# Optimization experiments

Hardware: AMD Instinct MI355X
Metric: run time of the kernel (lower is better)

The kernel has to match this reference:

```python
import jax, jax.numpy as jnp
import numpy as np

B, L, D = 4, 2048, 256
EXPAND, D_STATE, D_CONV = 2, 16, 4
D_INNER = EXPAND * D
DT_RANK = (D + 15) // 16  # ceil(d_model/16) = 16
N_HEADS = 4
H_MLP = int(D * 4.0)
EPS = 1e-5


def _ln(x, w, b):
    mu = x.mean(-1, keepdims=True)
    var = ((x - mu) ** 2).mean(-1, keepdims=True)
    return (x - mu) / jnp.sqrt(var + EPS) * w + b


def _silu(x):
    return x * jax.nn.sigmoid(x)


def _mamba(x, Win, convw, convb, Wx, Wdt, bdt, Alog, Dp, Wout):
    # x: (B, L, D) -> (B, L, D). Standard Mamba mixer (selective scan).
    b, l, d = x.shape
    xz = x @ Win.T                      # (b, l, 2*d_inner)
    xi, z = jnp.split(xz, 2, axis=-1)
    # depthwise causal conv1d, kernel D_CONV
    xc = jnp.swapaxes(xi, 1, 2)         # (b, d_inner, l)
    xc = jax.lax.conv_general_dilated(
        xc, convw, (1,), [(D_CONV - 1, 0)],
        feature_group_count=D_INNER, dimension_numbers=('NCW', 'OIW', 'NCW'))
    xi = _silu(jnp.swapaxes(xc + convb[None, :, None], 1, 2))  # (b, l, d_inner)
    dbl = xi @ Wx.T                     # (b, l, dt_rank + 2*d_state)
    dt = jax.nn.softplus(dbl[..., :DT_RANK] @ Wdt.T + bdt)     # (b, l, d_inner)
    Bm = dbl[..., DT_RANK:DT_RANK + D_STATE]                    # (b, l, n)
    Cm = dbl[..., DT_RANK + D_STATE:]                            # (b, l, n)
    A = -jnp.exp(Alog)                  # (d_inner, n)

    def step(h, ins):
        dt_t, B_t, C_t, u_t = ins       # (b,d_inner),(b,n),(b,n),(b,d_inner)
        h = h * jnp.exp(dt_t[..., None] * A) + dt_t[..., None] * B_t[:, None, :] * u_t[..., None]
        return h, jnp.einsum('bdn,bn->bd', h, C_t)

    xs = tuple(jnp.swapaxes(t, 0, 1) for t in (dt, Bm, Cm, xi))  # time-major
    h0 = jnp.zeros((b, D_INNER, D_STATE), x.dtype)
    _, ys = jax.lax.scan(step, h0, xs)  # ys: (l, b, d_inner)
    y = jnp.swapaxes(ys, 0, 1) + xi * Dp
    return (y * _silu(z)) @ Wout.T


def _attn(x, Wqkv, bqkv, Wo, bo):
    b, l, d = x.shape
    hd = d // N_HEADS
    qkv = x @ Wqkv.T + bqkv
    q, k, v = jnp.split(qkv, 3, axis=-1)
    sh = lambda t: t.reshape(b, l, N_HEADS, hd).transpose(0, 2, 1, 3)
    q, k, v = sh(q), sh(k), sh(v)
    a = jax.nn.softmax(jnp.einsum('bhqd,bhkd->bhqk', q, k) / np.float32(np.sqrt(hd)), axis=-1)
    o = jnp.einsum('bhqk,bhkd->bhqd', a, v).transpose(0, 2, 1, 3).reshape(b, l, d)
    return o @ Wo.T + bo


def setup_inputs() -> dict:
    key = jax.random.key(0)
    ks = iter(jax.random.split(key, 40))
    rn = lambda shape, s=0.02: jax.random.normal(next(ks), shape, jnp.float32) * s
    inp = {'x': jax.random.normal(next(ks), (B, L, D), jnp.float32)}
    for p in ('mf', 'mb'):
        inp[p + '_Win'] = rn((2 * D_INNER, D))
        inp[p + '_convw'] = rn((D_INNER, 1, D_CONV), 0.1)
        inp[p + '_convb'] = jnp.zeros((D_INNER,), jnp.float32)
        inp[p + '_Wx'] = rn((DT_RANK + 2 * D_STATE, D_INNER))
        inp[p + '_Wdt'] = rn((D_INNER, DT_RANK), 0.1)
        inp[p + '_bdt'] = rn((D_INNER,), 0.5)
        inp[p + '_Alog'] = jnp.log(jnp.broadcast_to(jnp.arange(1, D_STATE + 1, dtype=jnp.float32), (D_INNER, D_STATE)))
        inp[p + '_D'] = jnp.ones((D_INNER,), jnp.float32)
        inp[p + '_Wout'] = rn((D, D_INNER))
    for n in ('n1', 'n2', 'n3'):
        inp[n + 'w'] = jnp.ones((D,), jnp.float32)
        inp[n + 'b'] = jnp.zeros((D,), jnp.float32)
    inp['Wqkv'] = rn((3 * D, D))
    inp['bqkv'] = jnp.zeros((3 * D,), jnp.float32)
    inp['Wo'] = rn((D, D))
    inp['bo'] = jnp.zeros((D,), jnp.float32)
    inp['fc1w'] = rn((H_MLP, D))
    inp['fc1b'] = jnp.zeros((H_MLP,), jnp.float32)
    inp['fc2w'] = rn((D, H_MLP))
    inp['fc2b'] = jnp.zeros((D,), jnp.float32)
    return inp


def reference(x, n1w, n1b, n2w, n2b, n3w, n3b,
              mf_Win, mf_convw, mf_convb, mf_Wx, mf_Wdt, mf_bdt, mf_Alog, mf_D, mf_Wout,
              mb_Win, mb_convw, mb_convb, mb_Wx, mb_Wdt, mb_bdt, mb_Alog, mb_D, mb_Wout,
              Wqkv, bqkv, Wo, bo, fc1w, fc1b, fc2w, fc2b):
    # Mamba branch (bidirectional): DropPath is identity at eval
    h = _ln(x, n1w, n1b)
    fwd = _mamba(h, mf_Win, mf_convw, mf_convb, mf_Wx, mf_Wdt, mf_bdt, mf_Alog, mf_D, mf_Wout)
    bwd = jnp.flip(_mamba(jnp.flip(h, 1), mb_Win, mb_convw, mb_convb, mb_Wx, mb_Wdt, mb_bdt, mb_Alog, mb_D, mb_Wout), 1)
    x = x + fwd + bwd
    # Attention branch (full attention since window=None)
    x = x + _attn(_ln(x, n2w, n2b), Wqkv, bqkv, Wo, bo)
    # MLP branch (exact GELU like torch default)
    h = _ln(x, n3w, n3b)
    x = x + (jax.nn.gelu(h @ fc1w.T + fc1b, approximate=False) @ fc2w.T + fc2b)
    return x
```

## Files before the change

### kernel.cpp

```cpp
#include <hip/hip_runtime.h>
#include <hip/hip_bf16.h>
#include <math.h>

#define LL 2048
#define DD 256
#define MTOT 8192
#define DINNER 512
#define CT 32
#define NC 64

typedef __attribute__((ext_vector_type(8))) short short8;
typedef __attribute__((ext_vector_type(4))) float f32x4;

__device__ __forceinline__ float us2f(unsigned short u){
  return __uint_as_float(((unsigned)u) << 16);
}
__device__ __forceinline__ unsigned short f2us(float f){
  __hip_bfloat16 h = __float2bfloat16(f);
  return *(unsigned short*)&h;
}

__global__ void probe_kernel(const unsigned* __restrict__ alog, int* __restrict__ flag){
  if (threadIdx.x == 0 && blockIdx.x == 0) *flag = (alog[0] != 0u) ? 1 : 0;
}

struct Srcs { const void* p[32]; unsigned off[33]; unsigned foff[32]; };

__global__ __launch_bounds__(256) void cvt_all_kernel(Srcs s, float* __restrict__ dst,
                                                      unsigned short* __restrict__ db,
                                                      const int* __restrict__ flag,
                                                      unsigned total){
  unsigned i = blockIdx.x * 256u + threadIdx.x;
  if (i >= total) return;
  int k = 31;
  while (s.off[k] > i) --k;
  unsigned j = i - s.off[k];
  float v;
  if (*flag) v = us2f(((const unsigned short*)s.p[k])[j]);
  else       v = ((const float*)s.p[k])[j];
  if ((k == 24 && j < 65536u) || (k == 25 && j < 256u)) v *= 0.125f;
  db[i] = f2us(v);
  if (s.foff[k] != 0xFFFFFFFFu) dst[s.foff[k] + j] = v;
}

__global__ __launch_bounds__(256) void cvt_x_kernel(const void* __restrict__ src,
                                                    float* __restrict__ dst,
                                                    const int* __restrict__ flag, unsigned n){
  unsigned i = blockIdx.x * 256u + threadIdx.x;
  if (i >= n) return;
  if (*flag) dst[i] = us2f(((const unsigned short*)src)[i]);
  else       dst[i] = ((const float*)src)[i];
}

__global__ __launch_bounds__(256) void wc_prep_kernel(
    const float* __restrict__ Wdt, int dsWdt,
    const float* __restrict__ Wx, int dsWx,
    unsigned short* __restrict__ Wc)
{
  const unsigned g = blockIdx.x * 256u + threadIdx.x;
  const int dir = g >> 18;
  const unsigned idx = g & 262143u;
  const int n = idx >> 9, k = idx & 511;
  const float* wd = Wdt + (size_t)dir * dsWdt + n * 16;
  const float* wx = Wx + (size_t)dir * dsWx + k;
  float s = 0.f;
  #pragma unroll
  for (int j = 0; j < 16; ++j) s = fmaf(wd[j], wx[(size_t)j * 512], s);
  Wc[g] = f2us(s);
}

__global__ __launch_bounds__(256) void final_out_kernel(
    const float* __restrict__ xf, void* __restrict__ out,
    const int* __restrict__ flag, unsigned n)
{
  unsigned i = blockIdx.x * 256u + threadIdx.x;
  if (i >= n) return;
  float v = xf[i];
  if (*flag) ((unsigned short*)out)[i] = f2us(v);
  else       ((float*)out)[i] = v;
}

enum { G_BF16=0, G_GELU=1, G_RESID=2 };
__global__ __launch_bounds__(256) void gemm_mfma_kernel(
    const unsigned short* __restrict__ A, int lda, int agap,
    const unsigned short* __restrict__ W, const unsigned short* __restrict__ W2,
    int Kw, int nsplit, int ksplit,
    const float* __restrict__ bias,
    unsigned short* __restrict__ Cb, float* __restrict__ resid,
    int N, int K, int kslices, int mode)
{
  __shared__ unsigned short sA[64][40];
  __shared__ unsigned short sW[64][40];
  const int tid = threadIdx.x;
  const int w = tid >> 6, lane = tid & 63, quad = lane >> 4, l16 = lane & 15;
  const int m0 = blockIdx.y << 6, n0 = blockIdx.x << 6;
  const int ks = blockIdx.z;
  const int kper = K / kslices;
  const int srow = tid >> 2, skc = (tid & 3) << 3;
  int wr = n0 + srow;
  const unsigned short* Wbase = W;
  if (nsplit && wr >= nsplit){ Wbase = W2; wr -= nsplit; }
  f32x4 acc[4] = {};
  for (int k0 = ks * kper; k0 < ks * kper + kper; k0 += 32){
    int ac = k0 + skc;
    if (agap && ac >= 512) ac += 512;
    short8 av = *(const short8*)(A + (size_t)(m0 + srow) * lda + ac);
    int kk = k0 + skc;
    const unsigned short* Wp = Wbase;
    if (ksplit && kk >= ksplit){ Wp = W2; kk -= ksplit; }
    short8 wv = *(const short8*)(Wp + (size_t)wr * Kw + kk);
    __syncthreads();
    *(short8*)&sA[srow][skc] = av;
    *(short8*)&sW[srow][skc] = wv;
    __syncthreads();
    short8 af = *(const short8*)&sA[w * 16 + l16][quad << 3];
    #pragma unroll
    for (int ns = 0; ns < 4; ++ns){
      short8 wf = *(const short8*)&sW[ns * 16 + l16][quad << 3];
      acc[ns] = __builtin_amdgcn_mfma_f32_16x16x32_bf16(af, wf, acc[ns], 0, 0, 0);
    }
  }
  #pragma unroll
  for (int ns = 0; ns < 4; ++ns){
    const int n = n0 + ns * 16 + l16;
    const float bv = (bias && (mode != G_RESID || ks == 0)) ? bias[n] : 0.f;
    #pragma unroll
    for (int r = 0; r < 4; ++r){
      const int m = m0 + w * 16 + quad * 4 + r;
      const size_t off = (size_t)m * N + n;
      float v = acc[ns][r] + bv;
      if (mode == G_BF16) Cb[off] = f2us(v);
      else if (mode == G_GELU) Cb[off] = f2us(0.5f * v * (1.f + erff(v * 0.70710678118f)));
      else atomicAdd(resid + off, v);
    }
  }
}

__global__ __launch_bounds__(256) void dtbc_mfma_kernel(
    const unsigned short* __restrict__ xi,
    const unsigned short* __restrict__ Wc,
    const unsigned short* __restrict__ WxBCf,
    const unsigned short* __restrict__ WxBCb,
    const float* __restrict__ bdt0, int dsBdt,
    unsigned short* __restrict__ dt16,
    float* __restrict__ dblBC)
{
  __shared__ unsigned short sA[64][40];
  __shared__ unsigned short sW[64][40];
  const int tid = threadIdx.x;
  const int w = tid >> 6, lane = tid & 63, quad = lane >> 4, l16 = lane & 15;
  const int bx = blockIdx.x, m0 = blockIdx.y << 6, dir = blockIdx.z;
  const bool isBC = (bx == 8);
  const unsigned short* A = xi + (size_t)dir * 4194304;
  const unsigned short* W;
  if (isBC) W = dir ? WxBCb : WxBCf;
  else      W = Wc + (size_t)dir * 262144 + ((size_t)bx << 6) * 512;
  const int srow = tid >> 2, skc = (tid & 3) << 3;
  const int wrow = isBC ? (srow & 31) : srow;
  f32x4 acc[4] = {};
  for (int k0 = 0; k0 < 512; k0 += 32){
    short8 av = *(const short8*)(A + (size_t)(m0 + srow) * 512 + k0 + skc);
    short8 wv = *(const short8*)(W + (size_t)wrow * 512 + k0 + skc);
    __syncthreads();
    *(short8*)&sA[srow][skc] = av;
    *(short8*)&sW[srow][skc] = wv;
    __syncthreads();
    short8 af = *(const short8*)&sA[w * 16 + l16][quad << 3];
    #pragma unroll
    for (int ns = 0; ns < 4; ++ns){
      short8 wf = *(const short8*)&sW[ns * 16 + l16][quad << 3];
      acc[ns] = __builtin_amdgcn_mfma_f32_16x16x32_bf16(af, wf, acc[ns], 0, 0, 0);
    }
  }
  #pragma unroll
  for (int ns = 0; ns < 4; ++ns){
    const int nl = ns * 16 + l16;
    #pragma unroll
    for (int r = 0; r < 4; ++r){
      const int m = m0 + w * 16 + quad * 4 + r;
      float v = acc[ns][r];
      if (!isBC){
        const int n = (bx << 6) + nl;
        v += (bdt0 + (size_t)dir * dsBdt)[n];
        float sp = (v > 20.f) ? v : log1pf(__expf(v));
        dt16[(size_t)dir * 4194304 + (size_t)m * 512 + n] = f2us(sp);
      } else if (nl < 32){
        dblBC[(size_t)dir * 262144 + (size_t)m * 32 + nl] = v;
      }
    }
  }
}

__global__ __launch_bounds__(256) void ln_kernel(
    const float* __restrict__ xin,
    const float* __restrict__ w, const float* __restrict__ b,
    unsigned short* __restrict__ hout)
{
  const int row = blockIdx.x, tid = threadIdx.x;
  const size_t off = (size_t)row * DD + tid;
  float v = xin[off];
  float s = v, s2 = v * v;
  #pragma unroll
  for (int o = 32; o; o >>= 1){ s += __shfl_xor(s, o); s2 += __shfl_xor(s2, o); }
  __shared__ float ls[4], ls2[4];
  if ((tid & 63) == 0){ ls[tid >> 6] = s; ls2[tid >> 6] = s2; }
  __syncthreads();
  s  = ls[0] + ls[1] + ls[2] + ls[3];
  s2 = ls2[0] + ls2[1] + ls2[2] + ls2[3];
  const float mu  = s * (1.f / DD);
  const float var = s2 * (1.f / DD) - mu * mu;
  const float inv = rsqrtf(var + 1e-5f);
  hout[off] = f2us((v - mu) * inv * w[tid] + b[tid]);
}

__global__ __launch_bounds__(256) void conv_silu_kernel(
    const unsigned short* __restrict__ xzc, const float* __restrict__ convw0, int dsCw,
    const float* __restrict__ convb0, int dsCb, unsigned short* __restrict__ xi)
{
  const unsigned idx = blockIdx.x * 256u + threadIdx.x;
  const int c = idx & 511;
  const int t = (idx >> 9) & 2047;
  const int b = (idx >> 20) & 3;
  const int dir = idx >> 22;
  const float* cw = convw0 + (size_t)dir * dsCw;
  float acc = (convb0 + (size_t)dir * dsCb)[c];
  if (!dir){
    #pragma unroll
    for (int k = 0; k < 4; ++k){
      int tt = t - 3 + k;
      if (tt >= 0) acc += cw[c*4 + k] * us2f(xzc[((size_t)(b*2048 + tt))*2048 + c]);
    }
  } else {
    #pragma unroll
    for (int j = 0; j < 4; ++j){
      int tt = t + j;
      if (tt < 2048) acc += cw[c*4 + 3 - j] * us2f(xzc[((size_t)(b*2048 + tt))*2048 + 1024 + c]);
    }
  }
  xi[(size_t)dir * 4194304 + ((size_t)(b*2048 + t))*512 + c] = f2us(acc / (1.f + __expf(-acc)));
}

__global__ __launch_bounds__(256) void scan_part1_kernel(
    const unsigned short* __restrict__ dtb, int dsDt,
    const unsigned short* __restrict__ xib, int dsXi,
    const float* __restrict__ dblb, int dsDbl,
    const float* __restrict__ Alog, int dsAl,
    float* __restrict__ dtsum, int dsDts,
    float* __restrict__ hend, int dsHend)
{
  const int bx = blockIdx.x;
  const int dg = bx & 1, c = (bx >> 1) & (NC - 1), b = (bx >> 7) & 3, dir = bx >> 9;
  const int tid = threadIdx.x;
  const int d = dg * 256 + tid;
  const unsigned short* dt_ = dtb + (size_t)dir * dsDt;
  const unsigned short* xi_ = xib + (size_t)dir * dsXi;
  const float* db_ = dblb + (size_t)dir * dsDbl;
  const float* Al_ = Alog + (size_t)dir * dsAl;
  __shared__ float sB[CT][16];
  for (int i = tid; i < CT * 16; i += 256){
    const int s = i >> 4, nn = i & 15;
    const int t = dir ? (LL - 1 - (c * CT + s)) : (c * CT + s);
    sB[s][nn] = db_[(size_t)(b * LL + t) * 32 + nn];
  }
  float A[16];
  #pragma unroll
  for (int n = 0; n < 16; ++n) A[n] = -__expf(Al_[d * 16 + n]);
  __syncthreads();
  float h[16];
  #pragma unroll
  for (int n = 0; n < 16; ++n) h[n] = 0.f;
  float dts = 0.f;
  for (int s = 0; s < CT; ++s){
    const int t = dir ? (LL - 1 - (c * CT + s)) : (c * CT + s);
    const size_t row = (size_t)(b * LL + t);
    const float dtv = us2f(dt_[row * 512 + d]);
    const float uv  = us2f(xi_[row * 512 + d]);
    const float dtu = dtv * uv;
    dts += dtv;
    float bl[16];
    #pragma unroll
    for (int q = 0; q < 4; ++q) *(float4*)&bl[q * 4] = *(const float4*)&sB[s][q * 4];
    #pragma unroll
    for (int n = 0; n < 16; ++n){
      const float e = __expf(dtv * A[n]);
      h[n] = h[n] * e + dtu * bl[n];
    }
  }
  const size_t base = (size_t)dir * dsHend + ((size_t)((b * NC + c) * 512 + d)) * 16;
  #pragma unroll
  for (int q = 0; q < 4; ++q) *(float4*)&hend[base + q * 4] = *(const float4*)&h[q * 4];
  dtsum[(size_t)dir * dsDts + (size_t)(b * NC + c) * 512 + d] = dts;
}

__global__ __launch_bounds__(256) void scan_combine_kernel(
    const float* __restrict__ dtsum, int dsDts,
    float* __restrict__ hend, int dsHend,
    const float* __restrict__ Alog, int dsAl)
{
  const unsigned g = blockIdx.x * 256u + threadIdx.x;
  const int dir = g >> 15;
  const unsigned gg = g & 32767u;
  const int b = gg >> 13, d = (gg >> 4) & 511, n = gg & 15;
  const float A = -__expf((Alog + (size_t)dir * dsAl)[d * 16 + n]);
  const float* dts_ = dtsum + (size_t)dir * dsDts;
  float* he_ = hend + (size_t)dir * dsHend;
  float h = 0.f;
  for (int c = 0; c < NC; ++c){
    const size_t sb = ((size_t)((b * NC + c) * 512 + d)) * 16 + n;
    const float e = __expf(dts_[(size_t)(b * NC + c) * 512 + d] * A);
    const float he = he_[sb];
    he_[sb] = h;
    h = h * e + he;
  }
}

__global__ __launch_bounds__(256) void scan_part2_kernel(
    const unsigned short* __restrict__ dtb, int dsDt,
    const unsigned short* __restrict__ xib, int dsXi,
    const float* __restrict__ dblb, int dsDbl,
    unsigned short* __restrict__ xzc,
    const float* __restrict__ Alog, int dsAl,
    const float* __restrict__ Dp, int dsD,
    const float* __restrict__ hin, int dsHend)
{
  const int bx = blockIdx.x;
  const int dg = bx & 1, c = (bx >> 1) & (NC - 1), b = (bx >> 7) & 3, dir = bx >> 9;
  const int tid = threadIdx.x;
  const int d = dg * 256 + tid;
  const unsigned short* dt_ = dtb + (size_t)dir * dsDt;
  const unsigned short* xi_ = xib + (size_t)dir * dsXi;
  const float* db_ = dblb + (size_t)dir * dsDbl;
  const float* Al_ = Alog + (size_t)dir * dsAl;
  __shared__ float sB[CT][16];
  __shared__ float sC[CT][16];
  for (int i = tid; i < CT * 16; i += 256){
    const int s = i >> 4, nn = i & 15;
    const int t = dir ? (LL - 1 - (c * CT + s)) : (c * CT + s);
    sB[s][nn] = db_[(size_t)(b * LL + t) * 32 + nn];
    sC[s][nn] = db_[(size_t)(b * LL + t) * 32 + 16 + nn];
  }
  float A[16];
  #pragma unroll
  for (int n = 0; n < 16; ++n) A[n] = -__expf(Al_[d * 16 + n]);
  const float Dv = (Dp + (size_t)dir * dsD)[d];
  __syncthreads();
  float h[16];
  const size_t base = (size_t)dir * dsHend + ((size_t)((b * NC + c) * 512 + d)) * 16;
  #pragma unroll
  for (int q = 0; q < 4; ++q) *(float4*)&h[q * 4] = *(const float4*)&hin[base + q * 4];
  for (int s = 0; s < CT; ++s){
    const int t = dir ? (LL - 1 - (c * CT + s)) : (c * CT + s);
    const size_t row = (size_t)(b * LL + t);
    const float dtv = us2f(dt_[row * 512 + d]);
    const float uv  = us2f(xi_[row * 512 + d]);
    const float dtu = dtv * uv;
    float bl[16], cl[16];
    #pragma unroll
    for (int q = 0; q < 4; ++q){
      *(float4*)&bl[q * 4] = *(const float4*)&sB[s][q * 4];
      *(float4*)&cl[q * 4] = *(const float4*)&sC[s][q * 4];
    }
    float p = uv * Dv;
    #pragma unroll
    for (int n = 0; n < 16; ++n){
      const float e = __expf(dtv * A[n]);
      h[n] = h[n] * e + dtu * bl[n];
      p = fmaf(h[n], cl[n], p);
    }
    const float z = us2f(xzc[row * 2048 + dir * 1024 + 512 + d]);
    xzc[row * 2048 + dir * 1024 + d] = f2us(p * (z / (1.f + __expf(-z))));
  }
}

__global__ __launch_bounds__(256) void v_prep_kernel(
    const unsigned short* __restrict__ qkvb, unsigned short* __restrict__ Vt)
{
  const int kt = blockIdx.x;
  const int bh = blockIdx.y;
  const int b = bh >> 2, h = bh & 3;
  __shared__ unsigned short tile[64][72];
  #pragma unroll
  for (int rr = 0; rr < 4; ++rr){
    const int idx = (rr * 256 + threadIdx.x) * 4;
    const int key = idx >> 6, d = idx & 63;
    ushort4 v = *(const ushort4*)(qkvb + ((size_t)(b * 2048 + kt * 64 + key)) * 768 + 512 + h * 64 + d);
    *(ushort4*)&tile[key][d] = v;
  }
  __syncthreads();
  #pragma unroll
  for (int rr = 0; rr < 8; ++rr){
    const int o2 = rr * 256 + threadIdx.x;
    const int d = o2 >> 5, k2 = (o2 & 31) << 1;
    ushort2 u;
    u.x = tile[k2][d];
    u.y = tile[k2 + 1][d];
    *(ushort2*)(Vt + (size_t)bh * 131072 + (size_t)d * 2048 + kt * 64 + k2) = u;
  }
}

__global__ __launch_bounds__(256) void attn_mfma_kernel(
    const unsigned short* __restrict__ qkvb, const unsigned short* __restrict__ Vt,
    float* __restrict__ opart, float* __restrict__ lpart)
{
  __shared__ unsigned short sK[64][72];
  __shared__ unsigned short sV[64][72];
  __shared__ unsigned short sP[4][16][72];
  const int tid = threadIdx.x;
  const int w = tid >> 6, lane = tid & 63, quad = lane >> 4, l16 = lane & 15;
  const int bh = blockIdx.y;
  const int b = bh >> 2, h = bh & 3;
  const int q0 = blockIdx.x * 64;
  const int split = blockIdx.z;

  const unsigned short* qp = qkvb + ((size_t)(b * 2048 + q0 + w * 16 + l16)) * 768 + h * 64 + quad * 8;
  short8 qf0 = *(const short8*)qp;
  short8 qf1 = *(const short8*)(qp + 32);

  f32x4 o[4] = {{0,0,0,0},{0,0,0,0},{0,0,0,0},{0,0,0,0}};
  float lsum[4] = {0.f,0.f,0.f,0.f};

  const int kt0 = split * 1024;
  for (int kt = kt0; kt < kt0 + 1024; kt += 64){
    __syncthreads();
    #pragma unroll
    for (int r = 0; r < 2; ++r){
      const int idx = (r * 256 + tid) * 8;
      const int row = idx >> 6, c = idx & 63;
      *(short8*)&sK[row][c] = *(const short8*)(qkvb + ((size_t)(b * 2048 + kt + row)) * 768 + 256 + h * 64 + c);
      *(short8*)&sV[row][c] = *(const short8*)(Vt + (size_t)bh * 131072 + (size_t)row * 2048 + kt + c);
    }
    __syncthreads();

    float p[4][4];
    #pragma unroll
    for (int sub = 0; sub < 4; ++sub){
      short8 bk0 = *(const short8*)&sK[sub * 16 + l16][quad * 8];
      short8 bk1 = *(const short8*)&sK[sub * 16 + l16][32 + quad * 8];
      f32x4 acc = {0,0,0,0};
      acc = __builtin_amdgcn_mfma_f32_16x16x32_bf16(qf0, bk0, acc, 0, 0, 0);
      acc = __builtin_amdgcn_mfma_f32_16x16x32_bf16(qf1, bk1, acc, 0, 0, 0);
      #pragma unroll
      for (int r = 0; r < 4; ++r) p[sub][r] = __expf(acc[r]);
    }
    #pragma unroll
    for (int r = 0; r < 4; ++r)
      lsum[r] += p[0][r] + p[1][r] + p[2][r] + p[3][r];
    #pragma unroll
    for (int sub = 0; sub < 4; ++sub)
      #pragma unroll
      for (int r = 0; r < 4; ++r)
        sP[w][quad * 4 + r][sub * 16 + l16] = f2us(p[sub][r]);
    short8 pa0 = *(const short8*)&sP[w][l16][quad * 8];
    short8 pa1 = *(const short8*)&sP[w][l16][32 + quad * 8];
    #pragma unroll
    for (int nsub = 0; nsub < 4; ++nsub){
      short8 bv0 = *(const short8*)&sV[nsub * 16 + l16][quad * 8];
      short8 bv1 = *(const short8*)&sV[nsub * 16 + l16][32 + quad * 8];
      o[nsub] = __builtin_amdgcn_mfma_f32_16x16x32_bf16(pa0, bv0, o[nsub], 0, 0, 0);
      o[nsub] = __builtin_amdgcn_mfma_f32_16x16x32_bf16(pa1, bv1, o[nsub], 0, 0, 0);
    }
  }

  #pragma unroll
  for (int r = 0; r < 4; ++r){
    lsum[r] += __shfl_xor(lsum[r], 1); lsum[r] += __shfl_xor(lsum[r], 2);
    lsum[r] += __shfl_xor(lsum[r], 4); lsum[r] += __shfl_xor(lsum[r], 8);
  }
  const size_t obase = ((size_t)(split * 16 + bh)) * 2048;
  #pragma unroll
  for (int r = 0; r < 4; ++r){
    const int q = q0 + w * 16 + quad * 4 + r;
    #pragma unroll
    for (int nsub = 0; nsub < 4; ++nsub)
      opart[(obase + q) * 64 + nsub * 16 + l16] = o[nsub][r];
    if (l16 == 0) lpart[obase + q] = lsum[r];
  }
}

__global__ __launch_bounds__(256) void attn_merge_kernel(
    const float* __restrict__ opart, const float* __restrict__ lpart,
    unsigned short* __restrict__ outp)
{
  const unsigned g = blockIdx.x * 256u + threadIdx.x;
  const int d4 = (g & 15) << 2;
  const int q = (g >> 4) & 2047;
  const int bh = g >> 15;
  const size_t i0 = ((size_t)bh * 2048 + q) * 64 + d4;
  const size_t i1 = i0 + (size_t)16 * 2048 * 64;
  float4 o0 = *(const float4*)(opart + i0);
  float4 o1 = *(const float4*)(opart + i1);
  const float invl = 1.f / (lpart[bh * 2048 + q] + lpart[16 * 2048 + bh * 2048 + q]);
  const int b = bh >> 2, h = bh & 3;
  ushort4 u;
  u.x = f2us((o0.x + o1.x) * invl);
  u.y = f2us((o0.y + o1.y) * invl);
  u.z = f2us((o0.z + o1.z) * invl);
  u.w = f2us((o0.w + o1.w) * invl);
  *(ushort4*)(outp + ((size_t)(b * 2048 + q)) * 256 + h * 64 + d4) = u;
}

extern "C" void kernel_launch(void* const* d_in, const int* in_sizes, int n_in,
                              void* d_out, int out_size, void* d_ws, size_t ws_size,
                              hipStream_t stream)
{
  static const bool needf[33] = {
    false, false,true,true,true,true,true,true,true,false,
    false,true,true,true,true,true,true,true,false,
    true,true,true,true,true,true,
    false,true,false,true,false,true,false,true };

  int* flag  = (int*)d_ws;
  float* wts = (float*)d_ws + 16;

  Srcs srcs;
  unsigned acc = 0, facc = 0;
  unsigned foff_h[33];
  for (int i = 1; i <= 32; ++i){
    srcs.p[i - 1] = d_in[i];
    srcs.off[i - 1] = acc;
    acc += (unsigned)in_sizes[i];
    if (needf[i]){ srcs.foff[i - 1] = facc; foff_h[i] = facc; facc += (unsigned)in_sizes[i]; }
    else { srcs.foff[i - 1] = 0xFFFFFFFFu; foff_h[i] = 0xFFFFFFFFu; }
  }
  srcs.off[32] = acc;
  const unsigned wtotal = acc;
  const unsigned ftot = (facc + 3u) & ~3u;

  unsigned short* wb16 = (unsigned short*)(wts + ftot);
  float* xf    = wts + ftot + (wtotal + 1) / 2;
  float* xzc_f = xf + 2097152;
  float* xi_f  = xzc_f + 8388608;
  float* dblBC = xi_f + 4194304;
  float* hb_f  = dblBC + 524288;
  float* dt_f  = hb_f + 1048576;
  float* hend  = dt_f + 4194304;
  float* dtsum = hend + 4194304;
  float* wc_f  = dtsum + 262144;

  unsigned short* xzc  = (unsigned short*)xzc_f;
  unsigned short* xi16 = (unsigned short*)xi_f;
  unsigned short* hb16 = (unsigned short*)hb_f;
  unsigned short* dt16 = (unsigned short*)dt_f;
  unsigned short* Wc16 = (unsigned short*)wc_f;
  unsigned short* qkvb = xzc;
  unsigned short* Vt   = (unsigned short*)hend;
  float* opart = xi_f;
  float* lpart = dtsum;
  unsigned short* fc1o = xzc;

  auto wp  = [&](int i){ return wts + foff_h[i]; };
  auto wp16= [&](int i){ return wb16 + srcs.off[i - 1]; };

  hipLaunchKernelGGL(probe_kernel, dim3(1), dim3(64), 0, stream,
      (const unsigned*)d_in[7], flag);
  hipLaunchKernelGGL(cvt_all_kernel, dim3((wtotal + 255) / 256), dim3(256), 0, stream,
      srcs, wts, wb16, flag, wtotal);
  hipLaunchKernelGGL(cvt_x_kernel, dim3(MTOT * DD / 256), dim3(256), 0, stream,
      d_in[0], xf, flag, (unsigned)(MTOT * DD));

  const int dsCw = (int)(foff_h[11] - foff_h[2]);
  const int dsAl = (int)(foff_h[16] - foff_h[7]);
  const int dsD  = (int)(foff_h[17] - foff_h[8]);
  const int dsWx = (int)(foff_h[13] - foff_h[4]);
  const int dsWdt= (int)(foff_h[14] - foff_h[5]);
  const int dsBdt= (int)(foff_h[15] - foff_h[6]);
  const int dsCb2= (int)(foff_h[12] - foff_h[3]);

  hipLaunchKernelGGL(wc_prep_kernel, dim3(2048), dim3(256), 0, stream,
      wp(5), dsWdt, wp(4), dsWx, Wc16);

  auto gemm16 = [&](const unsigned short* Ab, int lda, int agap,
                    const unsigned short* W, const unsigned short* W2,
                    int Kw, int nsplit, int ksplit, const float* bias,
                    unsigned short* Cb, float* resid,
                    int N, int K, int ksl, int mode){
    hipLaunchKernelGGL(gemm_mfma_kernel, dim3(N / 64, MTOT / 64, ksl), dim3(256), 0, stream,
        Ab, lda, agap, W, W2, Kw, nsplit, ksplit, bias, Cb, resid, N, K, ksl, mode);
  };

  hipLaunchKernelGGL(ln_kernel, dim3(MTOT), dim3(256), 0, stream,
      xf, wp(19), wp(20), hb16);

  gemm16(hb16, 256, 0, wp16(1), wp16(10), 256, 1024, 0, nullptr,
         xzc, nullptr, 2048, 256, 1, G_BF16);
  hipLaunchKernelGGL(conv_silu_kernel, dim3(2 * MTOT * DINNER / 256), dim3(256), 0, stream,
      xzc, wp(2), dsCw, wp(3), dsCb2, xi16);
  hipLaunchKernelGGL(dtbc_mfma_kernel, dim3(9, MTOT / 64, 2), dim3(256), 0, stream,
      xi16, Wc16, wp16(4) + 8192, wp16(13) + 8192, wp(6), dsBdt, dt16, dblBC);
  hipLaunchKernelGGL(scan_part1_kernel, dim3(1024), dim3(256), 0, stream,
      dt16, 4194304, xi16, 4194304, dblBC, 262144, wp(7), dsAl,
      dtsum, 131072, hend, 2097152);
  hipLaunchKernelGGL(scan_combine_kernel, dim3(256), dim3(256), 0, stream,
      dtsum, 131072, hend, 2097152, wp(7), dsAl);
  hipLaunchKernelGGL(scan_part2_kernel, dim3(1024), dim3(256), 0, stream,
      dt16, 4194304, xi16, 4194304, dblBC, 262144, xzc, wp(7), dsAl,
      wp(8), dsD, hend, 2097152);
  gemm16(xzc, 2048, 1, wp16(9), wp16(18), 512, 0, 512, nullptr,
         nullptr, xf, 256, 1024, 2, G_RESID);

  hipLaunchKernelGGL(ln_kernel, dim3(MTOT), dim3(256), 0, stream,
      xf, wp(21), wp(22), hb16);
  gemm16(hb16, 256, 0, wp16(25), nullptr, 256, 0, 0, wp(26),
         qkvb, nullptr, 768, 256, 1, G_BF16);
  hipLaunchKernelGGL(v_prep_kernel, dim3(32, 16), dim3(256), 0, stream,
      qkvb, Vt);
  hipLaunchKernelGGL(attn_mfma_kernel, dim3(32, 16, 2), dim3(256), 0, stream,
      qkvb, Vt, opart, lpart);
  hipLaunchKernelGGL(attn_merge_kernel, dim3(2048), dim3(256), 0, stream,
      opart, lpart, hb16);
  gemm16(hb16, 256, 0, wp16(27), nullptr, 256, 0, 0, wp(28),
         nullptr, xf, 256, 256, 2, G_RESID);

  hipLaunchKernelGGL(ln_kernel, dim3(MTOT), dim3(256), 0, stream,
      xf, wp(23), wp(24), hb16);
  gemm16(hb16, 256, 0, wp16(29), nullptr, 256, 0, 0, wp(30),
         fc1o, nullptr, 1024, 256, 1, G_GELU);
  gemm16(fc1o, 1024, 0, wp16(31), nullptr, 1024, 0, 0, wp(32),
         nullptr, xf, 256, 1024, 2, G_RESID);
  hipLaunchKernelGGL(final_out_kernel, dim3(MTOT * DD / 256), dim3(256), 0, stream,
      xf, d_out, flag, (unsigned)(MTOT * DD));
}
```

Baseline: 513.5 us.

## Widen GEMM N-tiles so each block reuses the A tile across multiple W tiles

The GEMM kernel is templated on NT so each block computes 64 x (64*NT) outputs, loading the A tile once and reusing it across NT weight tiles. The dt/B/C projection kernel likewise computes three 64-column tiles per block. Several launches now use NT=2 or NT=4, and the out-projection and fc2 GEMMs raise their k-split count to keep enough blocks in the grid. This cuts redundant A loads and the number of blocks, at the cost of more registers and shared memory per block, and more atomics from the larger k-split.

```diff
diff --git a/kernel.cpp b/kernel.cpp
--- a/kernel.cpp
+++ b/kernel.cpp
@@ -81,7 +81,8 @@
 }
 
 enum { G_BF16=0, G_GELU=1, G_RESID=2 };
-__global__ __launch_bounds__(256) void gemm_mfma_kernel(
+template<int NT>
+__global__ __launch_bounds__(256) void gemm_nt_kernel(
     const unsigned short* __restrict__ A, int lda, int agap,
     const unsigned short* __restrict__ W, const unsigned short* __restrict__ W2,
     int Kw, int nsplit, int ksplit,
@@ -90,48 +91,59 @@
     int N, int K, int kslices, int mode)
 {
   __shared__ unsigned short sA[64][40];
-  __shared__ unsigned short sW[64][40];
+  __shared__ unsigned short sW[NT][64][40];
   const int tid = threadIdx.x;
   const int w = tid >> 6, lane = tid & 63, quad = lane >> 4, l16 = lane & 15;
-  const int m0 = blockIdx.y << 6, n0 = blockIdx.x << 6;
+  const int m0 = blockIdx.y << 6;
+  const int n0 = blockIdx.x * (NT << 6);
   const int ks = blockIdx.z;
   const int kper = K / kslices;
   const int srow = tid >> 2, skc = (tid & 3) << 3;
-  int wr = n0 + srow;
-  const unsigned short* Wbase = W;
-  if (nsplit && wr >= nsplit){ Wbase = W2; wr -= nsplit; }
-  f32x4 acc[4] = {};
+  const unsigned short* Arow = A + (size_t)(m0 + srow) * lda;
+  f32x4 acc[NT][4] = {};
   for (int k0 = ks * kper; k0 < ks * kper + kper; k0 += 32){
     int ac = k0 + skc;
     if (agap && ac >= 512) ac += 512;
-    short8 av = *(const short8*)(A + (size_t)(m0 + srow) * lda + ac);
-    int kk = k0 + skc;
-    const unsigned short* Wp = Wbase;
-    if (ksplit && kk >= ksplit){ Wp = W2; kk -= ksplit; }
-    short8 wv = *(const short8*)(Wp + (size_t)wr * Kw + kk);
+    short8 av = *(const short8*)(Arow + ac);
+    short8 wv[NT];
+    #pragma unroll
+    for (int nt = 0; nt < NT; ++nt){
+      int wr = n0 + (nt << 6) + srow;
+      const unsigned short* Wb = W;
+      if (nsplit && wr >= nsplit){ Wb = W2; wr -= nsplit; }
+      int kk = k0 + skc;
+      if (ksplit && kk >= ksplit){ Wb = W2; kk -= ksplit; }
+      wv[nt] = *(const short8*)(Wb + (size_t)wr * Kw + kk);
+    }
     __syncthreads();
     *(short8*)&sA[srow][skc] = av;
-    *(short8*)&sW[srow][skc] = wv;
+    #pragma unroll
+    for (int nt = 0; nt < NT; ++nt) *(short8*)&sW[nt][srow][skc] = wv[nt];
     __syncthreads();
     short8 af = *(const short8*)&sA[w * 16 + l16][quad << 3];
     #pragma unroll
+    for (int nt = 0; nt < NT; ++nt)
+      #pragma unroll
+      for (int ns = 0; ns < 4; ++ns){
+        short8 wf = *(const short8*)&sW[nt][ns * 16 + l16][quad << 3];
+        acc[nt][ns] = __builtin_amdgcn_mfma_f32_16x16x32_bf16(af, wf, acc[nt][ns], 0, 0, 0);
+      }
+  }
+  #pragma unroll
+  for (int nt = 0; nt < NT; ++nt){
+    #pragma unroll
     for (int ns = 0; ns < 4; ++ns){
-      short8 wf = *(const short8*)&sW[ns * 16 + l16][quad << 3];
-      acc[ns] = __builtin_amdgcn_mfma_f32_16x16x32_bf16(af, wf, acc[ns], 0, 0, 0);
-    }
-  }
-  #pragma unroll
-  for (int ns = 0; ns < 4; ++ns){
-    const int n = n0 + ns * 16 + l16;
-    const float bv = (bias && (mode != G_RESID || ks == 0)) ? bias[n] : 0.f;
-    #pragma unroll
-    for (int r = 0; r < 4; ++r){
-      const int m = m0 + w * 16 + quad * 4 + r;
-      const size_t off = (size_t)m * N + n;
-      float v = acc[ns][r] + bv;
-      if (mode == G_BF16) Cb[off] = f2us(v);
-      else if (mode == G_GELU) Cb[off] = f2us(0.5f * v * (1.f + erff(v * 0.70710678118f)));
-      else atomicAdd(resid + off, v);
+      const int n = n0 + (nt << 6) + ns * 16 + l16;
+      const float bv = (bias && (mode != G_RESID || ks == 0)) ? bias[n] : 0.f;
+      #pragma unroll
+      for (int r = 0; r < 4; ++r){
+        const int m = m0 + w * 16 + quad * 4 + r;
+        const size_t off = (size_t)m * N + n;
+        float v = acc[nt][ns][r] + bv;
+        if (mode == G_BF16) Cb[off] = f2us(v);
+        else if (mode == G_GELU) Cb[off] = f2us(0.5f * v * (1.f + erff(v * 0.70710678118f)));
+        else atomicAdd(resid + off, v);
+      }
     }
   }
 }
@@ -146,46 +158,57 @@
     float* __restrict__ dblBC)
 {
   __shared__ unsigned short sA[64][40];
-  __shared__ unsigned short sW[64][40];
+  __shared__ unsigned short sW[3][64][40];
   const int tid = threadIdx.x;
   const int w = tid >> 6, lane = tid & 63, quad = lane >> 4, l16 = lane & 15;
   const int bx = blockIdx.x, m0 = blockIdx.y << 6, dir = blockIdx.z;
-  const bool isBC = (bx == 8);
-  const unsigned short* A = xi + (size_t)dir * 4194304;
-  const unsigned short* W;
-  if (isBC) W = dir ? WxBCb : WxBCf;
-  else      W = Wc + (size_t)dir * 262144 + ((size_t)bx << 6) * 512;
   const int srow = tid >> 2, skc = (tid & 3) << 3;
-  const int wrow = isBC ? (srow & 31) : srow;
-  f32x4 acc[4] = {};
+  const unsigned short* Wp[3];
+  #pragma unroll
+  for (int jj = 0; jj < 3; ++jj){
+    const int j = bx * 3 + jj;
+    if (j < 8) Wp[jj] = Wc + (size_t)dir * 262144 + (size_t)(j * 64 + srow) * 512;
+    else       Wp[jj] = (dir ? WxBCb : WxBCf) + (size_t)(srow & 31) * 512;
+  }
+  const unsigned short* Arow = xi + (size_t)dir * 4194304 + (size_t)(m0 + srow) * 512;
+  f32x4 acc[3][4] = {};
   for (int k0 = 0; k0 < 512; k0 += 32){
-    short8 av = *(const short8*)(A + (size_t)(m0 + srow) * 512 + k0 + skc);
-    short8 wv = *(const short8*)(W + (size_t)wrow * 512 + k0 + skc);
+    short8 av = *(const short8*)(Arow + k0 + skc);
+    short8 wv[3];
+    #pragma unroll
+    for (int jj = 0; jj < 3; ++jj) wv[jj] = *(const short8*)(Wp[jj] + k0 + skc);
     __syncthreads();
     *(short8*)&sA[srow][skc] = av;
-    *(short8*)&sW[srow][skc] = wv;
+    #pragma unroll
+    for (int jj = 0; jj < 3; ++jj) *(short8*)&sW[jj][srow][skc] = wv[jj];
     __syncthreads();
     short8 af = *(const short8*)&sA[w * 16 + l16][quad << 3];
     #pragma unroll
+    for (int jj = 0; jj < 3; ++jj)
+      #pragma unroll
+      for (int ns = 0; ns < 4; ++ns){
+        short8 wf = *(const short8*)&sW[jj][ns * 16 + l16][quad << 3];
+        acc[jj][ns] = __builtin_amdgcn_mfma_f32_16x16x32_bf16(af, wf, acc[jj][ns], 0, 0, 0);
+      }
+  }
+  #pragma unroll
+  for (int jj = 0; jj < 3; ++jj){
+    const int j = bx * 3 + jj;
+    #pragma unroll
     for (int ns = 0; ns < 4; ++ns){
-      short8 wf = *(const short8*)&sW[ns * 16 + l16][quad << 3];
-      acc[ns] = __builtin_amdgcn_mfma_f32_16x16x32_bf16(af, wf, acc[ns], 0, 0, 0);
-    }
-  }
-  #pragma unroll
-  for (int ns = 0; ns < 4; ++ns){
-    const int nl = ns * 16 + l16;
-    #pragma unroll
-    for (int r = 0; r < 4; ++r){
-      const int m = m0 + w * 16 + quad * 4 + r;
-      float v = acc[ns][r];
-      if (!isBC){
-        const int n = (bx << 6) + nl;
-        v += (bdt0 + (size_t)dir * dsBdt)[n];
-        float sp = (v > 20.f) ? v : log1pf(__expf(v));
-        dt16[(size_t)dir * 4194304 + (size_t)m * 512 + n] = f2us(sp);
-      } else if (nl < 32){
-        dblBC[(size_t)dir * 262144 + (size_t)m * 32 + nl] = v;
+      const int nl = ns * 16 + l16;
+      #pragma unroll
+      for (int r = 0; r < 4; ++r){
+        const int m = m0 + w * 16 + quad * 4 + r;
+        float v = acc[jj][ns][r];
+        if (j < 8){
+          const int n = j * 64 + nl;
+          v += (bdt0 + (size_t)dir * dsBdt)[n];
+          float sp = (v > 20.f) ? v : log1pf(__expf(v));
+          dt16[(size_t)dir * 4194304 + (size_t)m * 512 + n] = f2us(sp);
+        } else if (nl < 32){
+          dblBC[(size_t)dir * 262144 + (size_t)m * 32 + nl] = v;
+        }
       }
     }
   }
@@ -569,23 +592,31 @@
   hipLaunchKernelGGL(wc_prep_kernel, dim3(2048), dim3(256), 0, stream,
       wp(5), dsWdt, wp(4), dsWx, Wc16);
 
-  auto gemm16 = [&](const unsigned short* Ab, int lda, int agap,
+  auto gemmNT = [&](int NT, const unsigned short* Ab, int lda, int agap,
                     const unsigned short* W, const unsigned short* W2,
                     int Kw, int nsplit, int ksplit, const float* bias,
                     unsigned short* Cb, float* resid,
                     int N, int K, int ksl, int mode){
-    hipLaunchKernelGGL(gemm_mfma_kernel, dim3(N / 64, MTOT / 64, ksl), dim3(256), 0, stream,
-        Ab, lda, agap, W, W2, Kw, nsplit, ksplit, bias, Cb, resid, N, K, ksl, mode);
+    dim3 grid(N / (64 * NT), MTOT / 64, ksl);
+    if (NT == 4)
+      hipLaunchKernelGGL(gemm_nt_kernel<4>, grid, dim3(256), 0, stream,
+          Ab, lda, agap, W, W2, Kw, nsplit, ksplit, bias, Cb, resid, N, K, ksl, mode);
+    else if (NT == 2)
+      hipLaunchKernelGGL(gemm_nt_kernel<2>, grid, dim3(256), 0, stream,
+          Ab, lda, agap, W, W2, Kw, nsplit, ksplit, bias, Cb, resid, N, K, ksl, mode);
+    else
+      hipLaunchKernelGGL(gemm_nt_kernel<1>, grid, dim3(256), 0, stream,
+          Ab, lda, agap, W, W2, Kw, nsplit, ksplit, bias, Cb, resid, N, K, ksl, mode);
   };
 
   hipLaunchKernelGGL(ln_kernel, dim3(MTOT), dim3(256), 0, stream,
       xf, wp(19), wp(20), hb16);
 
-  gemm16(hb16, 256, 0, wp16(1), wp16(10), 256, 1024, 0, nullptr,
+  gemmNT(4, hb16, 256, 0, wp16(1), wp16(10), 256, 1024, 0, nullptr,
          xzc, nullptr, 2048, 256, 1, G_BF16);
   hipLaunchKernelGGL(conv_silu_kernel, dim3(2 * MTOT * DINNER / 256), dim3(256), 0, stream,
       xzc, wp(2), dsCw, wp(3), dsCb2, xi16);
-  hipLaunchKernelGGL(dtbc_mfma_kernel, dim3(9, MTOT / 64, 2), dim3(256), 0, stream,
+  hipLaunchKernelGGL(dtbc_mfma_kernel, dim3(3, MTOT / 64, 2), dim3(256), 0, stream,
       xi16, Wc16, wp16(4) + 8192, wp16(13) + 8192, wp(6), dsBdt, dt16, dblBC);
   hipLaunchKernelGGL(scan_part1_kernel, dim3(1024), dim3(256), 0, stream,
       dt16, 4194304, xi16, 4194304, dblBC, 262144, wp(7), dsAl,
@@ -595,12 +626,12 @@
   hipLaunchKernelGGL(scan_part2_kernel, dim3(1024), dim3(256), 0, stream,
       dt16, 4194304, xi16, 4194304, dblBC, 262144, xzc, wp(7), dsAl,
       wp(8), dsD, hend, 2097152);
-  gemm16(xzc, 2048, 1, wp16(9), wp16(18), 512, 0, 512, nullptr,
-         nullptr, xf, 256, 1024, 2, G_RESID);
+  gemmNT(2, xzc, 2048, 1, wp16(9), wp16(18), 512, 0, 512, nullptr,
+         nullptr, xf, 256, 1024, 4, G_RESID);
 
   hipLaunchKernelGGL(ln_kernel, dim3(MTOT), dim3(256), 0, stream,
       xf, wp(21), wp(22), hb16);
-  gemm16(hb16, 256, 0, wp16(25), nullptr, 256, 0, 0, wp(26),
+  gemmNT(2, hb16, 256, 0, wp16(25), nullptr, 256, 0, 0, wp(26),
          qkvb, nullptr, 768, 256, 1, G_BF16);
   hipLaunchKernelGGL(v_prep_kernel, dim3(32, 16), dim3(256), 0, stream,
       qkvb, Vt);
@@ -608,15 +639,15 @@
       qkvb, Vt, opart, lpart);
   hipLaunchKernelGGL(attn_merge_kernel, dim3(2048), dim3(256), 0, stream,
       opart, lpart, hb16);
-  gemm16(hb16, 256, 0, wp16(27), nullptr, 256, 0, 0, wp(28),
+  gemmNT(2, hb16, 256, 0, wp16(27), nullptr, 256, 0, 0, wp(28),
          nullptr, xf, 256, 256, 2, G_RESID);
 
   hipLaunchKernelGGL(ln_kernel, dim3(MTOT), dim3(256), 0, stream,
       xf, wp(23), wp(24), hb16);
-  gemm16(hb16, 256, 0, wp16(29), nullptr, 256, 0, 0, wp(30),
+  gemmNT(2, hb16, 256, 0, wp16(29), nullptr, 256, 0, 0, wp(30),
          fc1o, nullptr, 1024, 256, 1, G_GELU);
-  gemm16(fc1o, 1024, 0, wp16(31), nullptr, 1024, 0, 0, wp(32),
-         nullptr, xf, 256, 1024, 2, G_RESID);
+  gemmNT(2, fc1o, 1024, 0, wp16(31), nullptr, 1024, 0, 0, wp(32),
+         nullptr, xf, 256, 1024, 4, G_RESID);
   hipLaunchKernelGGL(final_out_kernel, dim3(MTOT * DD / 256), dim3(256), 0, stream,
       xf, d_out, flag, (unsigned)(MTOT * DD));
 }
```

Measured after the change: 554.8 us. +8.0%, slower.

## Move all GEMMs to 128x128 MFMA tiles and merge dt/BC projection into it

Applied to the files above, without the earlier changes.

Replaces the 64x64 GEMM kernel with a 128x128 tile kernel in which each wave computes a 64x64 sub-tile (4x4 MFMA accumulators). This gives more reuse per LDS load and fewer global loads per FLOP. The separate dt/B/C projection kernel is folded into the same GEMM through a new G_DT mode. Its prep kernel now builds a combined 640-row weight matrix (the folded dt weights, the BC rows, then zero padding), which wastes some compute on the padded rows. The K-split for the residual GEMMs goes from 2 to 4 slices to keep enough blocks in flight, at the cost of more atomic adds and higher register pressure.

```diff
diff --git a/kernel.cpp b/kernel.cpp
--- a/kernel.cpp
+++ b/kernel.cpp
@@ -52,21 +52,25 @@
   else       dst[i] = ((const float*)src)[i];
 }
 
-__global__ __launch_bounds__(256) void wc_prep_kernel(
+__global__ __launch_bounds__(256) void wcfull_prep_kernel(
     const float* __restrict__ Wdt, int dsWdt,
     const float* __restrict__ Wx, int dsWx,
-    unsigned short* __restrict__ Wc)
+    unsigned short* __restrict__ Wf)
 {
   const unsigned g = blockIdx.x * 256u + threadIdx.x;
-  const int dir = g >> 18;
-  const unsigned idx = g & 262143u;
+  const int dir = g / 327680u;
+  const unsigned idx = g % 327680u;
   const int n = idx >> 9, k = idx & 511;
-  const float* wd = Wdt + (size_t)dir * dsWdt + n * 16;
-  const float* wx = Wx + (size_t)dir * dsWx + k;
-  float s = 0.f;
-  #pragma unroll
-  for (int j = 0; j < 16; ++j) s = fmaf(wd[j], wx[(size_t)j * 512], s);
-  Wc[g] = f2us(s);
+  float v = 0.f;
+  if (n < 512){
+    const float* wd = Wdt + (size_t)dir * dsWdt + n * 16;
+    const float* wx = Wx + (size_t)dir * dsWx + k;
+    #pragma unroll
+    for (int j = 0; j < 16; ++j) v = fmaf(wd[j], wx[(size_t)j * 512], v);
+  } else if (n < 544){
+    v = (Wx + (size_t)dir * dsWx)[(size_t)(16 + n - 512) * 512 + k];
+  }
+  Wf[(size_t)dir * 327680 + idx] = f2us(v);
 }
 
 __global__ __launch_bounds__(256) void final_out_kernel(
@@ -80,112 +84,95 @@
   else       ((float*)out)[i] = v;
 }
 
-enum { G_BF16=0, G_GELU=1, G_RESID=2 };
-__global__ __launch_bounds__(256) void gemm_mfma_kernel(
-    const unsigned short* __restrict__ A, int lda, int agap,
+enum { G_BF16=0, G_GELU=1, G_RESID=2, G_DT=3 };
+__global__ __launch_bounds__(256, 3) void gemm128_kernel(
+    const unsigned short* __restrict__ A, int lda, int agap, int dsA,
     const unsigned short* __restrict__ W, const unsigned short* __restrict__ W2,
-    int Kw, int nsplit, int ksplit,
-    const float* __restrict__ bias,
-    unsigned short* __restrict__ Cb, float* __restrict__ resid,
+    int Kw, int nsplit, int ksplit, int dsW,
+    const float* __restrict__ bias, int dsBias,
+    unsigned short* __restrict__ Cb, int dsCb,
+    float* __restrict__ resid, int dsResid,
+    const int* __restrict__ flag,
     int N, int K, int kslices, int mode)
 {
-  __shared__ unsigned short sA[64][40];
-  __shared__ unsigned short sW[64][40];
+  __shared__ unsigned short sA[128][40];
+  __shared__ unsigned short sW[128][40];
   const int tid = threadIdx.x;
   const int w = tid >> 6, lane = tid & 63, quad = lane >> 4, l16 = lane & 15;
-  const int m0 = blockIdx.y << 6, n0 = blockIdx.x << 6;
-  const int ks = blockIdx.z;
+  const int wm = w & 1, wn = w >> 1;
+  const int m0 = blockIdx.y << 7, n0 = blockIdx.x << 7;
+  const int bz = blockIdx.z;
+  const int dir = (mode == G_DT) ? bz : 0;
+  const int ks  = (mode == G_DT) ? 0 : bz;
   const int kper = K / kslices;
   const int srow = tid >> 2, skc = (tid & 3) << 3;
-  int wr = n0 + srow;
-  const unsigned short* Wbase = W;
-  if (nsplit && wr >= nsplit){ Wbase = W2; wr -= nsplit; }
-  f32x4 acc[4] = {};
+  const unsigned short* Aeff = A + (size_t)dir * dsA;
+  const unsigned short* Weff = W + (size_t)dir * dsW;
+
+  f32x4 acc[4][4] = {};
   for (int k0 = ks * kper; k0 < ks * kper + kper; k0 += 32){
     int ac = k0 + skc;
     if (agap && ac >= 512) ac += 512;
-    short8 av = *(const short8*)(A + (size_t)(m0 + srow) * lda + ac);
-    int kk = k0 + skc;
-    const unsigned short* Wp = Wbase;
-    if (ksplit && kk >= ksplit){ Wp = W2; kk -= ksplit; }
-    short8 wv = *(const short8*)(Wp + (size_t)wr * Kw + kk);
+    short8 a0 = *(const short8*)(Aeff + (size_t)(m0 + srow) * lda + ac);
+    short8 a1 = *(const short8*)(Aeff + (size_t)(m0 + 64 + srow) * lda + ac);
+    short8 w01[2];
+    #pragma unroll
+    for (int half = 0; half < 2; ++half){
+      int wr = n0 + (half << 6) + srow;
+      const unsigned short* Wb = Weff;
+      if (nsplit && wr >= nsplit){ Wb = W2; wr -= nsplit; }
+      int kk = k0 + skc;
+      if (ksplit && kk >= ksplit){ Wb = W2; kk -= ksplit; }
+      w01[half] = *(const short8*)(Wb + (size_t)wr * Kw + kk);
+    }
     __syncthreads();
-    *(short8*)&sA[srow][skc] = av;
-    *(short8*)&sW[srow][skc] = wv;
+    *(short8*)&sA[srow][skc] = a0;
+    *(short8*)&sA[64 + srow][skc] = a1;
+    *(short8*)&sW[srow][skc] = w01[0];
+    *(short8*)&sW[64 + srow][skc] = w01[1];
     __syncthreads();
-    short8 af = *(const short8*)&sA[w * 16 + l16][quad << 3];
-    #pragma unroll
-    for (int ns = 0; ns < 4; ++ns){
-      short8 wf = *(const short8*)&sW[ns * 16 + l16][quad << 3];
-      acc[ns] = __builtin_amdgcn_mfma_f32_16x16x32_bf16(af, wf, acc[ns], 0, 0, 0);
-    }
-  }
-  #pragma unroll
-  for (int ns = 0; ns < 4; ++ns){
-    const int n = n0 + ns * 16 + l16;
-    const float bv = (bias && (mode != G_RESID || ks == 0)) ? bias[n] : 0.f;
-    #pragma unroll
-    for (int r = 0; r < 4; ++r){
-      const int m = m0 + w * 16 + quad * 4 + r;
-      const size_t off = (size_t)m * N + n;
-      float v = acc[ns][r] + bv;
-      if (mode == G_BF16) Cb[off] = f2us(v);
-      else if (mode == G_GELU) Cb[off] = f2us(0.5f * v * (1.f + erff(v * 0.70710678118f)));
-      else atomicAdd(resid + off, v);
-    }
-  }
-}
-
-__global__ __launch_bounds__(256) void dtbc_mfma_kernel(
-    const unsigned short* __restrict__ xi,
-    const unsigned short* __restrict__ Wc,
-    const unsigned short* __restrict__ WxBCf,
-    const unsigned short* __restrict__ WxBCb,
-    const float* __restrict__ bdt0, int dsBdt,
-    unsigned short* __restrict__ dt16,
-    float* __restrict__ dblBC)
-{
-  __shared__ unsigned short sA[64][40];
-  __shared__ unsigned short sW[64][40];
-  const int tid = threadIdx.x;
-  const int w = tid >> 6, lane = tid & 63, quad = lane >> 4, l16 = lane & 15;
-  const int bx = blockIdx.x, m0 = blockIdx.y << 6, dir = blockIdx.z;
-  const bool isBC = (bx == 8);
-  const unsigned short* A = xi + (size_t)dir * 4194304;
-  const unsigned short* W;
-  if (isBC) W = dir ? WxBCb : WxBCf;
-  else      W = Wc + (size_t)dir * 262144 + ((size_t)bx << 6) * 512;
-  const int srow = tid >> 2, skc = (tid & 3) << 3;
-  const int wrow = isBC ? (srow & 31) : srow;
-  f32x4 acc[4] = {};
-  for (int k0 = 0; k0 < 512; k0 += 32){
-    short8 av = *(const short8*)(A + (size_t)(m0 + srow) * 512 + k0 + skc);
-    short8 wv = *(const short8*)(W + (size_t)wrow * 512 + k0 + skc);
-    __syncthreads();
-    *(short8*)&sA[srow][skc] = av;
-    *(short8*)&sW[srow][skc] = wv;
-    __syncthreads();
-    short8 af = *(const short8*)&sA[w * 16 + l16][quad << 3];
-    #pragma unroll
-    for (int ns = 0; ns < 4; ++ns){
-      short8 wf = *(const short8*)&sW[ns * 16 + l16][quad << 3];
-      acc[ns] = __builtin_amdgcn_mfma_f32_16x16x32_bf16(af, wf, acc[ns], 0, 0, 0);
-    }
-  }
-  #pragma unroll
-  for (int ns = 0; ns < 4; ++ns){
-    const int nl = ns * 16 + l16;
-    #pragma unroll
-    for (int r = 0; r < 4; ++r){
-      const int m = m0 + w * 16 + quad * 4 + r;
-      float v = acc[ns][r];
-      if (!isBC){
-        const int n = (bx << 6) + nl;
-        v += (bdt0 + (size_t)dir * dsBdt)[n];
-        float sp = (v > 20.f) ? v : log1pf(__expf(v));
-        dt16[(size_t)dir * 4194304 + (size_t)m * 512 + n] = f2us(sp);
-      } else if (nl < 32){
-        dblBC[(size_t)dir * 262144 + (size_t)m * 32 + nl] = v;
+    short8 af[4], wf[4];
+    #pragma unroll
+    for (int i = 0; i < 4; ++i){
+      af[i] = *(const short8*)&sA[wm * 64 + i * 16 + l16][quad << 3];
+      wf[i] = *(const short8*)&sW[wn * 64 + i * 16 + l16][quad << 3];
+    }
+    #pragma unroll
+    for (int i = 0; i < 4; ++i)
+      #pragma unroll
+      for (int j = 0; j < 4; ++j)
+        acc[i][j] = __builtin_amdgcn_mfma_f32_16x16x32_bf16(af[i], wf[j], acc[i][j], 0, 0, 0);
+  }
+
+  const float* biasEff = bias ? bias + (size_t)dir * dsBias : nullptr;
+  #pragma unroll
+  for (int j = 0; j < 4; ++j){
+    const int n = n0 + wn * 64 + j * 16 + l16;
+    float bv = 0.f;
+    if (biasEff){
+      if (mode == G_DT){ if (n < 512) bv = biasEff[n]; }
+      else if (mode != G_RESID || ks == 0) bv = biasEff[n];
+    }
+    #pragma unroll
+    for (int i = 0; i < 4; ++i){
+      #pragma unroll
+      for (int r = 0; r < 4; ++r){
+        const int m = m0 + wm * 64 + i * 16 + quad * 4 + r;
+        float v = acc[i][j][r] + bv;
+        if (mode == G_BF16){
+          Cb[(size_t)m * N + n] = f2us(v);
+        } else if (mode == G_GELU){
+          Cb[(size_t)m * N + n] = f2us(0.5f * v * (1.f + erff(v * 0.70710678118f)));
+        } else if (mode == G_RESID){
+          atomicAdd(resid + (size_t)m * N + n, v);
+        } else {
+          if (n < 512){
+            float sp = (v > 20.f) ? v : log1pf(__expf(v));
+            (Cb + (size_t)dir * dsCb)[(size_t)m * 512 + n] = f2us(sp);
+          } else if (n < 544){
+            (resid + (size_t)dir * dsResid)[(size_t)m * 32 + (n - 512)] = v;
+          }
+        }
       }
     }
   }
@@ -541,7 +528,7 @@
   unsigned short* xi16 = (unsigned short*)xi_f;
   unsigned short* hb16 = (unsigned short*)hb_f;
   unsigned short* dt16 = (unsigned short*)dt_f;
-  unsigned short* Wc16 = (unsigned short*)wc_f;
+  unsigned short* Wfull= (unsigned short*)wc_f;
   unsigned short* qkvb = xzc;
   unsigned short* Vt   = (unsigned short*)hend;
   float* opart = xi_f;
@@ -566,27 +553,30 @@
   const int dsBdt= (int)(foff_h[15] - foff_h[6]);
   const int dsCb2= (int)(foff_h[12] - foff_h[3]);
 
-  hipLaunchKernelGGL(wc_prep_kernel, dim3(2048), dim3(256), 0, stream,
-      wp(5), dsWdt, wp(4), dsWx, Wc16);
-
-  auto gemm16 = [&](const unsigned short* Ab, int lda, int agap,
-                    const unsigned short* W, const unsigned short* W2,
-                    int Kw, int nsplit, int ksplit, const float* bias,
-                    unsigned short* Cb, float* resid,
-                    int N, int K, int ksl, int mode){
-    hipLaunchKernelGGL(gemm_mfma_kernel, dim3(N / 64, MTOT / 64, ksl), dim3(256), 0, stream,
-        Ab, lda, agap, W, W2, Kw, nsplit, ksplit, bias, Cb, resid, N, K, ksl, mode);
+  hipLaunchKernelGGL(wcfull_prep_kernel, dim3(2560), dim3(256), 0, stream,
+      wp(5), dsWdt, wp(4), dsWx, Wfull);
+
+  auto gemm128 = [&](const unsigned short* Ab, int lda, int agap, int dsA,
+                     const unsigned short* W, const unsigned short* W2,
+                     int Kw, int nsplit, int ksplit, int dsW,
+                     const float* bias, int dsBias,
+                     unsigned short* Cb, int dsCb, float* resid, int dsResid,
+                     int N, int K, int nz, int mode){
+    dim3 grid(N / 128, MTOT / 128, nz);
+    hipLaunchKernelGGL(gemm128_kernel, grid, dim3(256), 0, stream,
+        Ab, lda, agap, dsA, W, W2, Kw, nsplit, ksplit, dsW, bias, dsBias,
+        Cb, dsCb, resid, dsResid, flag, N, K, nz, mode);
   };
 
   hipLaunchKernelGGL(ln_kernel, dim3(MTOT), dim3(256), 0, stream,
       xf, wp(19), wp(20), hb16);
 
-  gemm16(hb16, 256, 0, wp16(1), wp16(10), 256, 1024, 0, nullptr,
-         xzc, nullptr, 2048, 256, 1, G_BF16);
+  gemm128(hb16, 256, 0, 0, wp16(1), wp16(10), 256, 1024, 0, 0,
+          nullptr, 0, xzc, 0, nullptr, 0, 2048, 256, 1, G_BF16);
   hipLaunchKernelGGL(conv_silu_kernel, dim3(2 * MTOT * DINNER / 256), dim3(256), 0, stream,
       xzc, wp(2), dsCw, wp(3), dsCb2, xi16);
-  hipLaunchKernelGGL(dtbc_mfma_kernel, dim3(9, MTOT / 64, 2), dim3(256), 0, stream,
-      xi16, Wc16, wp16(4) + 8192, wp16(13) + 8192, wp(6), dsBdt, dt16, dblBC);
+  gemm128(xi16, 512, 0, 4194304, Wfull, nullptr, 512, 0, 0, 327680,
+          wp(6), dsBdt, dt16, 4194304, dblBC, 262144, 640, 512, 2, G_DT);
   hipLaunchKernelGGL(scan_part1_kernel, dim3(1024), dim3(256), 0, stream,
       dt16, 4194304, xi16, 4194304, dblBC, 262144, wp(7), dsAl,
       dtsum, 131072, hend, 2097152);
@@ -595,28 +585,28 @@
   hipLaunchKernelGGL(scan_part2_kernel, dim3(1024), dim3(256), 0, stream,
       dt16, 4194304, xi16, 4194304, dblBC, 262144, xzc, wp(7), dsAl,
       wp(8), dsD, hend, 2097152);
-  gemm16(xzc, 2048, 1, wp16(9), wp16(18), 512, 0, 512, nullptr,
-         nullptr, xf, 256, 1024, 2, G_RESID);
+  gemm128(xzc, 2048, 1, 0, wp16(9), wp16(18), 512, 0, 512, 0,
+          nullptr, 0, nullptr, 0, xf, 0, 256, 1024, 4, G_RESID);
 
   hipLaunchKernelGGL(ln_kernel, dim3(MTOT), dim3(256), 0, stream,
       xf, wp(21), wp(22), hb16);
-  gemm16(hb16, 256, 0, wp16(25), nullptr, 256, 0, 0, wp(26),
-         qkvb, nullptr, 768, 256, 1, G_BF16);
+  gemm128(hb16, 256, 0, 0, wp16(25), nullptr, 256, 0, 0, 0,
+          wp(26), 0, qkvb, 0, nullptr, 0, 768, 256, 1, G_BF16);
   hipLaunchKernelGGL(v_prep_kernel, dim3(32, 16), dim3(256), 0, stream,
       qkvb, Vt);
   hipLaunchKernelGGL(attn_mfma_kernel, dim3(32, 16, 2), dim3(256), 0, stream,
       qkvb, Vt, opart, lpart);
   hipLaunchKernelGGL(attn_merge_kernel, dim3(2048), dim3(256), 0, stream,
       opart, lpart, hb16);
-  gemm16(hb16, 256, 0, wp16(27), nullptr, 256, 0, 0, wp(28),
-         nullptr, xf, 256, 256, 2, G_RESID);
+  gemm128(hb16, 256, 0, 0, wp16(27), nullptr, 256, 0, 0, 0,
+          wp(28), 0, nullptr, 0, xf, 0, 256, 256, 2, G_RESID);
 
   hipLaunchKernelGGL(ln_kernel, dim3(MTOT), dim3(256), 0, stream,
       xf, wp(23), wp(24), hb16);
-  gemm16(hb16, 256, 0, wp16(29), nullptr, 256, 0, 0, wp(30),
-         fc1o, nullptr, 1024, 256, 1, G_GELU);
-  gemm16(fc1o, 1024, 0, wp16(31), nullptr, 1024, 0, 0, wp(32),
-         nullptr, xf, 256, 1024, 2, G_RESID);
+  gemm128(hb16, 256, 0, 0, wp16(29), nullptr, 256, 0, 0, 0,
+          wp(30), 0, fc1o, 0, nullptr, 0, 1024, 256, 1, G_GELU);
+  gemm128(fc1o, 1024, 0, 0, wp16(31), nullptr, 1024, 0, 0, 0,
+          nullptr, 0, nullptr, 0, xf, 0, 256, 1024, 4, G_RESID);
   hipLaunchKernelGGL(final_out_kernel, dim3(MTOT * DD / 256), dim3(256), 0, stream,
       xf, d_out, flag, (unsigned)(MTOT * DD));
 }
```

New measurement: 587.3 us. 1.14x slower.
